# Optimization experiments

Hardware: AMD Instinct MI355X
Metric: run time of the kernel (lower is better)

Reference implementation:

```python
import jax, jax.numpy as jnp
import numpy as np

D_MODEL = 1024
H = 16
D_K = D_MODEL // H  # 64


def setup_inputs() -> dict:
    key = jax.random.key(0)
    ks = jax.random.split(key, 10)
    s = 1.0 / np.sqrt(D_MODEL)
    x = jax.random.normal(ks[0], (4, 2048, D_MODEL), dtype=jnp.float32)
    # Per-head linear weights stacked: [H, d_model, d_k]
    Wq = jax.random.uniform(ks[1], (H, D_MODEL, D_K), jnp.float32, -s, s)
    bq = jax.random.uniform(ks[2], (H, D_K), jnp.float32, -s, s)
    Wk = jax.random.uniform(ks[3], (H, D_MODEL, D_K), jnp.float32, -s, s)
    bk = jax.random.uniform(ks[4], (H, D_K), jnp.float32, -s, s)
    Wv = jax.random.uniform(ks[5], (H, D_MODEL, D_K), jnp.float32, -s, s)
    bv = jax.random.uniform(ks[6], (H, D_K), jnp.float32, -s, s)
    so = 1.0 / np.sqrt(H * D_K)
    Wo = jax.random.uniform(ks[7], (H * D_K, D_MODEL), jnp.float32, -so, so)
    bo = jax.random.uniform(ks[8], (D_MODEL,), jnp.float32, -so, so)
    return {"x": x, "Wq": Wq, "bq": bq, "Wk": Wk, "bk": bk, "Wv": Wv, "bv": bv, "Wo": Wo, "bo": bo}


def reference(x, Wq, bq, Wk, bk, Wv, bv, Wo, bo):
    # x: [B, S, D]; Wq/Wk/Wv: [H, D, d_k]; b*: [H, d_k]
    q = jnp.einsum('bsd,hdk->bhsk', x, Wq) + bq[None, :, None, :]
    k = jnp.einsum('bsd,hdk->bhsk', x, Wk) + bk[None, :, None, :]
    v = jnp.einsum('bsd,hdk->bhsk', x, Wv) + bv[None, :, None, :]
    scores = jnp.einsum('bhqk,bhsk->bhqs', q, k) / np.sqrt(D_K)
    S = x.shape[1]
    causal = jnp.triu(jnp.ones((S, S), dtype=bool), k=1)  # True above diagonal
    scores = jnp.where(causal, -jnp.inf, scores)
    attn = jax.nn.softmax(scores, axis=-1)
    ctx = jnp.einsum('bhqs,bhsk->bhqk', attn, v)  # [B, H, S, d_k]
    B = x.shape[0]
    # concat heads: torch cats head outputs along last dim -> [B, S, H*d_k]
    ctx = jnp.transpose(ctx, (0, 2, 1, 3)).reshape(B, S, H * D_K)
    return ctx @ Wo + bo
```

## Files before the change

### kernel.cpp

```cpp
#include <hip/hip_runtime.h>
#include <hip/hip_bf16.h>

typedef unsigned short u16;
typedef __attribute__((ext_vector_type(8))) short short8;
typedef __attribute__((ext_vector_type(4))) short short4v;
typedef __attribute__((ext_vector_type(4))) float floatx4;

#define D_MODEL 1024
#define NH 16
#define SEQ 2048
#define BATCH 4
#define M_ROWS 8192
#define N_QKV 3072
#define PS_LD 72

__device__ __forceinline__ u16 f2u(float f) {
    __hip_bfloat16 h = __float2bfloat16(f);
    u16 u; __builtin_memcpy(&u, &h, 2); return u;
}

__device__ __forceinline__ void async_copy16(const u16* g, u16* l) {
    __builtin_amdgcn_global_load_lds(
        (const __attribute__((address_space(1))) unsigned int*)(g),
        (__attribute__((address_space(3))) unsigned int*)(l),
        16, 0, 0);
}

__global__ __launch_bounds__(256) void prep(
    const float* __restrict__ x,
    const float* __restrict__ Wq, const float* __restrict__ Wk,
    const float* __restrict__ Wv, const float* __restrict__ Wo,
    const float* __restrict__ bq, const float* __restrict__ bk,
    const float* __restrict__ bv, const float* __restrict__ bo,
    u16* __restrict__ xb, u16* __restrict__ Wpt, u16* __restrict__ Wot,
    float* __restrict__ biasp)
{
    __shared__ u16 T[64 * 72];
    const int tid = threadIdx.x;
    const int blk = blockIdx.x;

    if (blk < 4096) {
        size_t i = ((size_t)blk * 256 + tid) * 8;
        float4 f0 = *(const float4*)&x[i];
        float4 f1 = *(const float4*)&x[i + 4];
        u16 t[8] = {f2u(f0.x), f2u(f0.y), f2u(f0.z), f2u(f0.w),
                    f2u(f1.x), f2u(f1.y), f2u(f1.z), f2u(f1.w)};
        *(short8*)&xb[i] = *(short8*)t;
        return;
    }
    if (blk == 5120) {
        #pragma unroll
        for (int j = 0; j < 16; j++) {
            int idx = j * 256 + tid;
            float v;
            if (idx < 1024)      v = bq[idx] * 0.125f;
            else if (idx < 2048) v = bk[idx - 1024];
            else if (idx < 3072) v = bv[idx - 2048];
            else                 v = bo[idx - 3072];
            biasp[idx] = v;
        }
        return;
    }
    const int wb = blk - 4096;
    const int r = tid >> 2, s4 = (tid & 3) * 16;
    if (wb < 768) {
        int sel = wb / 256, rem = wb % 256;
        int h = rem >> 4, ktile = rem & 15;
        const float* W = (sel == 0) ? Wq : ((sel == 1) ? Wk : Wv);
        const float scale = (sel == 0) ? 0.125f : 1.0f;
        const float* src = W + ((size_t)h * 1024 + ktile * 64 + r) * 64 + s4;
        #pragma unroll
        for (int i = 0; i < 16; i++) T[(s4 + i) * 72 + r] = f2u(src[i] * scale);
        __syncthreads();
        u16 tmp[16];
        #pragma unroll
        for (int i = 0; i < 16; i++) tmp[i] = T[r * 72 + s4 + i];
        u16* dst = Wpt + ((size_t)sel * 1024 + h * 64 + r) * 1024 + ktile * 64 + s4;
        *(short8*)&dst[0] = *(short8*)&tmp[0];
        *(short8*)&dst[8] = *(short8*)&tmp[8];
    } else {
        int rem = wb - 768;
        int nt = rem >> 4, kt2 = rem & 15;
        const float* src = Wo + ((size_t)kt2 * 64 + r) * 1024 + nt * 64 + s4;
        #pragma unroll
        for (int i = 0; i < 16; i++) T[(s4 + i) * 72 + r] = f2u(src[i]);
        __syncthreads();
        u16 tmp[16];
        #pragma unroll
        for (int i = 0; i < 16; i++) tmp[i] = T[r * 72 + s4 + i];
        u16* dst = Wot + ((size_t)nt * 64 + r) * 1024 + kt2 * 64 + s4;
        *(short8*)&dst[0] = *(short8*)&tmp[0];
        *(short8*)&dst[8] = *(short8*)&tmp[8];
    }
}

__global__ __launch_bounds__(256) void vtrans(const u16* __restrict__ QKV,
                                              u16* __restrict__ Vtg) {
    __shared__ u16 T[64 * 72];
    const int bh = blockIdx.x, kt = blockIdx.y;
    const int b = bh >> 4, h = bh & 15;
    const int tid = threadIdx.x;
    const int r = tid >> 2, s4 = (tid & 3) * 16;
    const u16* vp = QKV + (size_t)(b * SEQ + kt * 64 + r) * N_QKV + 2 * D_MODEL + h * 64 + s4;
    *(short8*)&T[r * 72 + s4]     = *(const short8*)&vp[0];
    *(short8*)&T[r * 72 + s4 + 8] = *(const short8*)&vp[8];
    __syncthreads();
    u16 tmp[16];
    #pragma unroll
    for (int i = 0; i < 16; i++) tmp[i] = T[(s4 + i) * 72 + r];
    u16* op = Vtg + ((size_t)bh * 64 + r) * SEQ + kt * 64 + s4;
    *(short8*)&op[0] = *(short8*)&tmp[0];
    *(short8*)&op[8] = *(short8*)&tmp[8];
}

template <typename OT>
__global__ __launch_bounds__(256) void gemm128(
    const u16* __restrict__ A, const u16* __restrict__ Bt,
    const float* __restrict__ bias, OT* __restrict__ C,
    int M, int N, int K)
{
    __shared__ u16 As[128 * 64];
    __shared__ u16 Bs[128 * 64];
    const int tid = threadIdx.x;
    const int w = tid >> 6, lane = tid & 63;
    const int l16 = lane & 15, quad = lane >> 4;
    const int bn = blockIdx.x * 128, bm = blockIdx.y * 128;
    const int wr = (w >> 1) * 64, wc = (w & 1) * 64;

    floatx4 acc[4][4];
    #pragma unroll
    for (int i = 0; i < 4; i++)
        #pragma unroll
        for (int j = 0; j < 4; j++) acc[i][j] = (floatx4){0.f, 0.f, 0.f, 0.f};

    for (int k0 = 0; k0 < K; k0 += 64) {
        #pragma unroll
        for (int c = 0; c < 4; c++) {
            const int off = (w * 4 + c) * 1024 + lane * 16;
            const int row = off >> 7, seg = (off >> 4) & 7;
            async_copy16(A  + (size_t)(bm + row) * K + k0 + seg * 8, &As[(w * 4 + c) * 512]);
            async_copy16(Bt + (size_t)(bn + row) * K + k0 + seg * 8, &Bs[(w * 4 + c) * 512]);
        }
        __syncthreads();
        #pragma unroll
        for (int kc = 0; kc < 2; kc++) {
            short8 a[4], b[4];
            #pragma unroll
            for (int i = 0; i < 4; i++)
                a[i] = *(short8*)&As[(wr + i * 16 + l16) * 64 + kc * 32 + quad * 8];
            #pragma unroll
            for (int i = 0; i < 4; i++)
                b[i] = *(short8*)&Bs[(wc + i * 16 + l16) * 64 + kc * 32 + quad * 8];
            #pragma unroll
            for (int mm = 0; mm < 4; mm++)
                #pragma unroll
                for (int nn = 0; nn < 4; nn++)
                    acc[mm][nn] = __builtin_amdgcn_mfma_f32_16x16x32_bf16(
                        a[mm], b[nn], acc[mm][nn], 0, 0, 0);
        }
        __syncthreads();
    }

    #pragma unroll
    for (int nn = 0; nn < 4; nn++) {
        const int col = bn + wc + nn * 16 + l16;
        const float bi = bias[col];
        #pragma unroll
        for (int mm = 0; mm < 4; mm++) {
            const int row = bm + wr + mm * 16 + quad * 4;
            #pragma unroll
            for (int r = 0; r < 4; r++) {
                float v = acc[mm][nn][r] + bi;
                if constexpr (sizeof(OT) == 2) ((u16*)C)[(size_t)(row + r) * N + col] = f2u(v);
                else                           C[(size_t)(row + r) * N + col] = v;
            }
        }
    }
}

__global__ __launch_bounds__(256) void attn_mfma(
    const u16* __restrict__ QKV, const u16* __restrict__ Vtg, u16* __restrict__ ctx)
{
    __shared__ u16 Ks[2][64 * 64];
    __shared__ u16 Vs[2][64 * 64];
    __shared__ u16 Ps[128 * PS_LD];

    const int bh = blockIdx.x;
    const int qt = (int)(gridDim.y - 1) - (int)blockIdx.y;
    const int b = bh >> 4, h = bh & 15;
    const int tid = threadIdx.x;
    const int w = tid >> 6, lane = tid & 63;
    const int l16 = lane & 15, quad = lane >> 4;

    const int r0 = tid >> 3,        c0 = tid & 7;
    const int r1 = (256 + tid) >> 3, c1 = tid & 7;
    const int sw0 = c0 ^ (r0 & 7), sw1 = c1 ^ (r1 & 7);

    short8 q[2][2];
    #pragma unroll
    for (int m = 0; m < 2; m++) {
        const u16* qp = QKV + (size_t)(b * SEQ + qt * 128 + w * 32 + m * 16 + l16) * N_QKV + h * 64;
        q[m][0] = *(const short8*)&qp[quad * 8];
        q[m][1] = *(const short8*)&qp[32 + quad * 8];
    }

    floatx4 O[2][4];
    #pragma unroll
    for (int m = 0; m < 2; m++)
        #pragma unroll
        for (int i = 0; i < 4; i++) O[m][i] = (floatx4){0.f, 0.f, 0.f, 0.f};
    float li[2] = {0.f, 0.f};

    const int nkt = 2 * qt + 2;
    const int qrow_w_max = qt * 128 + w * 32 + 31;

    const size_t kbase = (size_t)(b * SEQ) * N_QKV + D_MODEL + h * 64;
    const size_t vbase = (size_t)bh * 64 * SEQ;

    {
        float4 ka = *(const float4*)(QKV + kbase + (size_t)(0 + r0) * N_QKV + c0 * 8);
        float4 kb = *(const float4*)(QKV + kbase + (size_t)(0 + r1) * N_QKV + c1 * 8);
        float4 va = *(const float4*)(Vtg + vbase + (size_t)r0 * SEQ + 0 + c0 * 8);
        float4 vb = *(const float4*)(Vtg + vbase + (size_t)r1 * SEQ + 0 + c1 * 8);
        *(float4*)&Ks[0][r0 * 64 + sw0 * 8] = ka;
        *(float4*)&Ks[0][r1 * 64 + sw1 * 8] = kb;
        *(float4*)&Vs[0][r0 * 64 + sw0 * 8] = va;
        *(float4*)&Vs[0][r1 * 64 + sw1 * 8] = vb;
    }
    __syncthreads();

    for (int kt = 0; kt < nkt; kt++) {
        const int buf = kt & 1;
        const bool pre = (kt + 1 < nkt);
        float4 ka, kb, va, vb;
        if (pre) {
            const int t1 = (kt + 1) * 64;
            ka = *(const float4*)(QKV + kbase + (size_t)(t1 + r0) * N_QKV + c0 * 8);
            kb = *(const float4*)(QKV + kbase + (size_t)(t1 + r1) * N_QKV + c1 * 8);
            va = *(const float4*)(Vtg + vbase + (size_t)r0 * SEQ + t1 + c0 * 8);
            vb = *(const float4*)(Vtg + vbase + (size_t)r1 * SEQ + t1 + c1 * 8);
        }

        if (kt * 64 <= qrow_w_max) {
            short8 kf[4][2];
            #pragma unroll
            for (int ns = 0; ns < 4; ns++) {
                const int rr = ns * 16 + l16, rs = rr & 7;
                kf[ns][0] = *(short8*)&Ks[buf][rr * 64 + (quad ^ rs) * 8];
                kf[ns][1] = *(short8*)&Ks[buf][rr * 64 + ((4 + quad) ^ rs) * 8];
            }
            const bool needMask = (kt * 64 + 63 > qt * 128 + w * 32);

            #pragma unroll
            for (int m = 0; m < 2; m++) {
                floatx4 z[4];
                #pragma unroll
                for (int ns = 0; ns < 4; ns++) {
                    floatx4 t = (floatx4){0.f, 0.f, 0.f, 0.f};
                    t = __builtin_amdgcn_mfma_f32_16x16x32_bf16(kf[ns][0], q[m][0], t, 0, 0, 0);
                    t = __builtin_amdgcn_mfma_f32_16x16x32_bf16(kf[ns][1], q[m][1], t, 0, 0, 0);
                    z[ns] = t;
                }
                const int qrow_g = qt * 128 + w * 32 + m * 16 + l16;
                const int prow = (w * 32 + m * 16 + l16) * PS_LD;
                float sum = 0.f;
                #pragma unroll
                for (int ns = 0; ns < 4; ns++) {
                    u16 pk[4];
                    #pragma unroll
                    for (int r = 0; r < 4; r++) {
                        float s = z[ns][r];
                        const int key = kt * 64 + ns * 16 + quad * 4 + r;
                        if (needMask && key > qrow_g) s = -INFINITY;
                        float p = __expf(s - 8.0f);
                        pk[r] = f2u(p);
                        sum += p;
                    }
                    *(short4v*)&Ps[prow + ns * 16 + quad * 4] = *(short4v*)pk;
                }
                sum += __shfl_xor(sum, 16);
                sum += __shfl_xor(sum, 32);
                li[m] += sum;
            }

            short8 vf[4][2];
            #pragma unroll
            for (int ds = 0; ds < 4; ds++) {
                const int rr = ds * 16 + l16, rs = rr & 7;
                vf[ds][0] = *(short8*)&Vs[buf][rr * 64 + (quad ^ rs) * 8];
                vf[ds][1] = *(short8*)&Vs[buf][rr * 64 + ((4 + quad) ^ rs) * 8];
            }
            #pragma unroll
            for (int m = 0; m < 2; m++) {
                const int prow = (w * 32 + m * 16 + l16) * PS_LD;
                short8 p0 = *(short8*)&Ps[prow + quad * 8];
                short8 p1 = *(short8*)&Ps[prow + 32 + quad * 8];
                #pragma unroll
                for (int ds = 0; ds < 4; ds++) {
                    O[m][ds] = __builtin_amdgcn_mfma_f32_16x16x32_bf16(vf[ds][0], p0, O[m][ds], 0, 0, 0);
                    O[m][ds] = __builtin_amdgcn_mfma_f32_16x16x32_bf16(vf[ds][1], p1, O[m][ds], 0, 0, 0);
                }
            }
        }

        if (pre) {
            const int nb = buf ^ 1;
            *(float4*)&Ks[nb][r0 * 64 + sw0 * 8] = ka;
            *(float4*)&Ks[nb][r1 * 64 + sw1 * 8] = kb;
            *(float4*)&Vs[nb][r0 * 64 + sw0 * 8] = va;
            *(float4*)&Vs[nb][r1 * 64 + sw1 * 8] = vb;
        }
        __syncthreads();
    }

    #pragma unroll
    for (int m = 0; m < 2; m++) {
        const float inv = 1.0f / li[m];
        const size_t base = (size_t)(b * SEQ + qt * 128 + w * 32 + m * 16 + l16) * D_MODEL + h * 64;
        #pragma unroll
        for (int ds = 0; ds < 4; ds++) {
            u16 o[4];
            #pragma unroll
            for (int r = 0; r < 4; r++) o[r] = f2u(O[m][ds][r] * inv);
            *(short4v*)&ctx[base + ds * 16 + quad * 4] = *(short4v*)o;
        }
    }
}

extern "C" void kernel_launch(void* const* d_in, const int* in_sizes, int n_in,
                              void* d_out, int out_size, void* d_ws, size_t ws_size,
                              hipStream_t stream) {
    const float* x  = (const float*)d_in[0];
    const float* Wq = (const float*)d_in[1];
    const float* bq = (const float*)d_in[2];
    const float* Wk = (const float*)d_in[3];
    const float* bk = (const float*)d_in[4];
    const float* Wv = (const float*)d_in[5];
    const float* bv = (const float*)d_in[6];
    const float* Wo = (const float*)d_in[7];
    const float* bo = (const float*)d_in[8];
    float* out = (float*)d_out;

    char* ws = (char*)d_ws;
    float* biasp = (float*)ws;
    u16*   Wpt   = (u16*)(ws + 0x10000);
    u16*   Wot   = (u16*)(ws + 0x620000);
    u16*   xb    = (u16*)(ws + 0x840000);
    u16*   Vtg   = xb;
    u16*   QKV   = (u16*)(ws + 0x1840000);
    u16*   ctx   = (u16*)(ws + 0x4840000);

    prep<<<5121, 256, 0, stream>>>(x, Wq, Wk, Wv, Wo, bq, bk, bv, bo,
                                   xb, Wpt, Wot, biasp);

    gemm128<u16><<<dim3(N_QKV / 128, M_ROWS / 128), 256, 0, stream>>>(
        xb, Wpt, biasp, QKV, M_ROWS, N_QKV, D_MODEL);

    vtrans<<<dim3(64, 32), 256, 0, stream>>>(QKV, Vtg);

    attn_mfma<<<dim3(BATCH * NH, SEQ / 128), 256, 0, stream>>>(QKV, Vtg, ctx);

    gemm128<float><<<dim3(D_MODEL / 128, M_ROWS / 128), 256, 0, stream>>>(
        ctx, Wot, biasp + N_QKV, out, M_ROWS, D_MODEL, D_MODEL);
}
```

Measured before the change: 293.7 us.

## Add 256x256-tile 8-wave pipelined GEMM for the QKV projection

Adds a new gemm256 kernel with 256x256 output tiles, 512 threads (8 waves), XOR-swizzled LDS staging via async global-to-LDS copies, and a four-phase interleaved schedule that overlaps loads with MFMA work and raises priority during the MFMA phases. The QKV projection GEMM now uses it instead of the 128x128 kernel. The larger tile raises data reuse per LDS byte and cuts global traffic. In exchange it uses 128 KB of LDS per block and many accumulator registers, and the grid shrinks to 12x32 blocks, which may reduce occupancy or leave CUs unevenly loaded.

```diff
diff --git a/kernel.cpp b/kernel.cpp
--- a/kernel.cpp
+++ b/kernel.cpp
@@ -171,6 +171,150 @@
             #pragma unroll
             for (int r = 0; r < 4; r++) {
                 float v = acc[mm][nn][r] + bi;
+                if constexpr (sizeof(OT) == 2) ((u16*)C)[(size_t)(row + r) * N + col] = f2u(v);
+                else                           C[(size_t)(row + r) * N + col] = v;
+            }
+        }
+    }
+}
+
+#define G256_BAR   __builtin_amdgcn_s_barrier()
+#define G256_LGKM0 { asm volatile("s_waitcnt lgkmcnt(0)" ::: "memory"); \
+                     __builtin_amdgcn_sched_barrier(0); }
+
+#define G256_STG(dstbase, s0, s1) { \
+    async_copy16((s0), &lds[(dstbase) + stw]); \
+    async_copy16((s1), &lds[(dstbase) + 4096 + stw]); }
+
+#define G256_STAGE_A(bb, half, kq) \
+    G256_STG((bb) * 32768 + (half) * 8192, \
+             pA[0] + (size_t)(half) * hstep + (kq), \
+             pA[1] + (size_t)(half) * hstep + (kq))
+
+#define G256_STAGE_B(bb, half, kq) \
+    G256_STG((bb) * 32768 + 16384 + (half) * 8192, \
+             pB[0] + (size_t)(half) * hstep + (kq), \
+             pB[1] + (size_t)(half) * hstep + (kq))
+
+#define G256_LDA4(dst, bb, mi0) { \
+    const int _b = (bb) * 32768 + wm * 8192; \
+    _Pragma("unroll") \
+    for (int mi = 0; mi < 4; mi++) { \
+        const int _r = _b + (((mi0) + mi) * 16 + l16) * 64; \
+        dst[mi * 2]     = *(const short8*)&lds[_r + col0]; \
+        dst[mi * 2 + 1] = *(const short8*)&lds[_r + col1]; \
+    } }
+
+#define G256_LDB2(dst, bb, ni0) { \
+    const int _b = (bb) * 32768 + 16384 + (wn >> 1) * 8192 + (wn & 1) * 4096; \
+    _Pragma("unroll") \
+    for (int ni = 0; ni < 2; ni++) { \
+        const int _r = _b + (((ni0) + ni) * 16 + l16) * 64; \
+        dst[ni * 2]     = *(const short8*)&lds[_r + col0]; \
+        dst[ni * 2 + 1] = *(const short8*)&lds[_r + col1]; \
+    } }
+
+#define G256_MMA8(av, bv, MI0, NI0) { \
+    _Pragma("unroll") \
+    for (int mi = 0; mi < 4; mi++) \
+    _Pragma("unroll") \
+    for (int ni = 0; ni < 2; ni++) { \
+        acc[(MI0) + mi][(NI0) + ni] = __builtin_amdgcn_mfma_f32_16x16x32_bf16( \
+            av[mi * 2],     bv[ni * 2],     acc[(MI0) + mi][(NI0) + ni], 0, 0, 0); \
+        acc[(MI0) + mi][(NI0) + ni] = __builtin_amdgcn_mfma_f32_16x16x32_bf16( \
+            av[mi * 2 + 1], bv[ni * 2 + 1], acc[(MI0) + mi][(NI0) + ni], 0, 0, 0); \
+    } }
+
+template <typename OT>
+__global__ __launch_bounds__(512, 2) void gemm256(
+    const u16* __restrict__ A, const u16* __restrict__ Bt,
+    const float* __restrict__ bias, OT* __restrict__ C,
+    int M, int N, int K)
+{
+    __shared__ u16 lds[65536];
+    const int tid = threadIdx.x;
+    const int w = tid >> 6, lane = tid & 63;
+    const int l16 = lane & 15, quad = lane >> 4;
+    const int wm = w >> 2, wn = w & 3;
+    const int bn = blockIdx.x * 256, bm = blockIdx.y * 256;
+
+    const u16* pA[2]; const u16* pB[2];
+    #pragma unroll
+    for (int j = 0; j < 2; j++) {
+        const int d = (j * 512 + tid) * 16;
+        const int s = d ^ (((d >> 7) & 7) << 4);
+        const int r = s >> 7;
+        const int c = (s & 127) >> 1;
+        pA[j] = A  + (size_t)(bm + r) * K + c;
+        pB[j] = Bt + (size_t)(bn + r) * K + c;
+    }
+    const size_t hstep = (size_t)128 * K;
+    const int stw = w * 512;
+
+    const int xm = (l16 & 7) << 3;
+    const int col0 = (quad * 8) ^ xm;
+    const int col1 = (32 + quad * 8) ^ xm;
+
+    floatx4 acc[8][4];
+    #pragma unroll
+    for (int i = 0; i < 8; i++)
+        #pragma unroll
+        for (int j = 0; j < 4; j++) acc[i][j] = (floatx4){0.f, 0.f, 0.f, 0.f};
+
+    G256_STAGE_A(0, 0, 0);  G256_STAGE_A(0, 1, 0);
+    G256_STAGE_B(0, 0, 0);  G256_STAGE_B(0, 1, 0);
+    G256_STAGE_B(1, 0, 64); G256_STAGE_B(1, 1, 64);
+    asm volatile("s_waitcnt vmcnt(0)" ::: "memory");
+    __syncthreads();
+
+    short8 aL[8], aH[8], bL[4], bH[4];
+    const int NKT = K >> 6;
+    for (int kt = 0; kt < NKT; ++kt) {
+        const int buf = kt & 1, nb = buf ^ 1;
+        const int kqA = (kt + 1) << 6, kqB = (kt + 2) << 6;
+        const bool stA = (kt + 1 < NKT), stB = (kt + 2 < NKT);
+
+        G256_LDA4(aL, buf, 0);
+        G256_LDB2(bL, buf, 0);
+        if (stA) { G256_STAGE_A(nb, 0, kqA); }
+        asm volatile("s_waitcnt lgkmcnt(8)" ::: "memory");
+        G256_BAR; G256_LGKM0;
+        __builtin_amdgcn_s_setprio(1); G256_MMA8(aL, bL, 0, 0);
+        __builtin_amdgcn_s_setprio(0); G256_BAR;
+
+        G256_LDB2(bH, buf, 2);
+        if (stA) { G256_STAGE_A(nb, 1, kqA); }
+        G256_BAR; G256_LGKM0;
+        __builtin_amdgcn_s_setprio(1); G256_MMA8(aL, bH, 0, 2);
+        __builtin_amdgcn_s_setprio(0); G256_BAR;
+
+        G256_LDA4(aH, buf, 4);
+        if (stB) { G256_STAGE_B(buf, 0, kqB); }
+        G256_BAR; G256_LGKM0;
+        __builtin_amdgcn_s_setprio(1); G256_MMA8(aH, bH, 4, 2);
+        __builtin_amdgcn_s_setprio(0); G256_BAR;
+
+        if (stB) {
+            G256_STAGE_B(buf, 1, kqB);
+            asm volatile("s_waitcnt vmcnt(4)" ::: "memory");
+        } else if (stA) {
+            asm volatile("s_waitcnt vmcnt(0)" ::: "memory");
+        }
+        G256_BAR;
+        __builtin_amdgcn_s_setprio(1); G256_MMA8(aH, bL, 4, 0);
+        __builtin_amdgcn_s_setprio(0); G256_BAR;
+    }
+
+    #pragma unroll
+    for (int ni = 0; ni < 4; ni++) {
+        const int col = bn + wn * 64 + ni * 16 + l16;
+        const float bi = bias[col];
+        #pragma unroll
+        for (int mi = 0; mi < 8; mi++) {
+            const int row = bm + wm * 128 + mi * 16 + quad * 4;
+            #pragma unroll
+            for (int r = 0; r < 4; r++) {
+                float v = acc[mi][ni][r] + bi;
                 if constexpr (sizeof(OT) == 2) ((u16*)C)[(size_t)(row + r) * N + col] = f2u(v);
                 else                           C[(size_t)(row + r) * N + col] = v;
             }
@@ -353,7 +497,7 @@
     prep<<<5121, 256, 0, stream>>>(x, Wq, Wk, Wv, Wo, bq, bk, bv, bo,
                                    xb, Wpt, Wot, biasp);
 
-    gemm128<u16><<<dim3(N_QKV / 128, M_ROWS / 128), 256, 0, stream>>>(
+    gemm256<u16><<<dim3(N_QKV / 256, M_ROWS / 256), 512, 0, stream>>>(
         xb, Wpt, biasp, QKV, M_ROWS, N_QKV, D_MODEL);
 
     vtrans<<<dim3(64, 32), 256, 0, stream>>>(QKV, Vtg);
```

Result: faster. 286.2 us (-2.6%).
